# Performance work log

Measured on AMD Instinct MI355X. Metric: run time of the kernel, lower is better.

## Reference

```python
import jax, jax.numpy as jnp
import numpy as np

NUM_HEADS = 16

def setup_inputs() -> dict:
    key = jax.random.key(0)
    ks = jax.random.split(key, 5)
    N, T, D = 16, 4096, 1024
    # Linear weights stored as (in, out): y = x @ W + b (equivalent to torch x @ W.T + b)
    return {
        "x": jax.random.normal(ks[0], (N, T, D), jnp.float32),
        "w_qkv": jax.random.normal(ks[1], (D, 3 * D), jnp.float32) * (D ** -0.5),
        "b_qkv": jax.random.normal(ks[2], (3 * D,), jnp.float32) * 0.02,
        "w_proj": jax.random.normal(ks[3], (D, D), jnp.float32) * (D ** -0.5),
        "b_proj": jax.random.normal(ks[4], (D,), jnp.float32) * 0.02,
    }

def reference(x, w_qkv, b_qkv, w_proj, b_proj):
    N, T, D = x.shape
    H = NUM_HEADS
    hd = D // H
    scale = hd ** -0.5
    qkv = x @ w_qkv + b_qkv                      # (N,T,3D)
    qkv = qkv.reshape(N, T, 3, H, hd)
    q, k, v = qkv[:, :, 0], qkv[:, :, 1], qkv[:, :, 2]   # each (N,T,H,hd)
    # Faithful to source: matmul over last two dims -> scores across HEADS, (N,T,H,H)
    attn = jnp.einsum('nthd,ntgd->nthg', q * scale, k)
    attn = jax.nn.softmax(attn, axis=-1)
    out = jnp.einsum('nthg,ntgd->nthd', attn, v)         # (N,T,H,hd)
    # Faithful: transpose(2,1) then flatten -> (N,H,T,hd).reshape(N,T,D)
    out = out.transpose(0, 2, 1, 3).reshape(N, T, D)
    return out @ w_proj + b_proj
```

## Files before the change

### kernel.cpp

```cpp
#include <hip/hip_runtime.h>
#include <hip/hip_bf16.h>
#include <stdint.h>

typedef __bf16 bf16x8 __attribute__((ext_vector_type(8)));
typedef float f32x4 __attribute__((ext_vector_type(4)));
typedef unsigned short us8 __attribute__((ext_vector_type(8)));

__device__ __forceinline__ float bf2f(unsigned short u) {
    return __uint_as_float(((unsigned)u) << 16);
}
__device__ __forceinline__ unsigned short f2bf(float f) {
    __bf16 b = (__bf16)f;
    return __builtin_bit_cast(unsigned short, b);
}

__device__ __forceinline__ void gload16(const char* g, char* l) {
    __builtin_amdgcn_global_load_lds(
        (const __attribute__((address_space(1))) void*)g,
        (__attribute__((address_space(3))) void*)l, 16, 0, 0);
}

__global__ __launch_bounds__(256) void transpose_cast(
    const float* __restrict__ in, unsigned short* __restrict__ out,
    int K, int N)
{
    __shared__ float tile[32][33];
    const int tx = threadIdx.x, ty = threadIdx.y;
    const int n0 = blockIdx.x * 32, k0 = blockIdx.y * 32;
    #pragma unroll
    for (int i = 0; i < 32; i += 8)
        tile[ty + i][tx] = in[(long)(k0 + ty + i) * N + n0 + tx];
    __syncthreads();
    #pragma unroll
    for (int i = 0; i < 32; i += 8)
        out[(long)(n0 + ty + i) * K + k0 + tx] = f2bf(tile[tx][ty + i]);
}

__global__ __launch_bounds__(256) void cast_f32_bf16(
    const float* __restrict__ in, unsigned short* __restrict__ out, long n)
{
    const long stride = (long)gridDim.x * 256 * 8;
    for (long i = ((long)blockIdx.x * 256 + threadIdx.x) * 8; i < n; i += stride) {
        const f32x4 u0 = *(const f32x4*)&in[i];
        const f32x4 u1 = *(const f32x4*)&in[i + 4];
        us8 w;
        #pragma unroll
        for (int e = 0; e < 4; ++e) { w[e] = f2bf(u0[e]); w[e + 4] = f2bf(u1[e]); }
        *(us8*)&out[i] = w;
    }
}

#define MFMA16x16(a, b, c) __builtin_amdgcn_mfma_f32_16x16x32_bf16(a, b, c, 0, 0, 0)

#define PHASE_SYNC_PRE()                          \
    __builtin_amdgcn_sched_barrier(0);            \
    __builtin_amdgcn_s_barrier();                 \
    asm volatile("s_waitcnt lgkmcnt(0)");         \
    __builtin_amdgcn_sched_barrier(0);            \
    __builtin_amdgcn_s_setprio(1);

#define PHASE_SYNC_POST()                         \
    __builtin_amdgcn_s_setprio(0);                \
    __builtin_amdgcn_sched_barrier(0);            \
    __builtin_amdgcn_s_barrier();

#define TILE_BODY(T, BUFOFF)                                                     \
  do {                                                                           \
    const bool doStage = ((T) + 2 < KT);                                         \
    const long gk = (long)((T) + 2) * 128;                                       \
    bf16x8 alo[4][2], ahi[4][2], blo[2][2], bhi[2][2];                           \
                             \
    _Pragma("unroll")                                                            \
    for (int mi = 0; mi < 4; ++mi) {                                             \
        alo[mi][0] = *(const bf16x8*)(smem + (BUFOFF) + aBase + mi*2048 + k0);   \
        alo[mi][1] = *(const bf16x8*)(smem + (BUFOFF) + aBase + mi*2048 + k1);   \
    }                                                                            \
    _Pragma("unroll")                                                            \
    for (int ni = 0; ni < 2; ++ni) {                                             \
        blo[ni][0] = *(const bf16x8*)(smem + (BUFOFF) + bBase + ni*2048 + k0);   \
        blo[ni][1] = *(const bf16x8*)(smem + (BUFOFF) + bBase + ni*2048 + k1);   \
    }                                                                            \
    PHASE_SYNC_PRE()                                                             \
    _Pragma("unroll")                                                            \
    for (int mi = 0; mi < 4; ++mi)                                               \
        _Pragma("unroll")                                                        \
        for (int ni = 0; ni < 2; ++ni) {                                         \
            acc[mi][ni] = MFMA16x16(alo[mi][0], blo[ni][0], acc[mi][ni]);        \
            acc[mi][ni] = MFMA16x16(alo[mi][1], blo[ni][1], acc[mi][ni]);        \
        }                                                                        \
    PHASE_SYNC_POST()                                                            \
                     \
    _Pragma("unroll")                                                            \
    for (int mi = 0; mi < 4; ++mi) {                                             \
        ahi[mi][0] = *(const bf16x8*)(smem + (BUFOFF) + aBase + 8192 + mi*2048 + k0); \
        ahi[mi][1] = *(const bf16x8*)(smem + (BUFOFF) + aBase + 8192 + mi*2048 + k1); \
    }                                                                            \
    if (doStage) {                                                               \
        gload16(aStage + (long)(0*64)*Kb + gk, smem + (BUFOFF) + 0*8192 + ldsW); \
        gload16(aStage + (long)(2*64)*Kb + gk, smem + (BUFOFF) + 2*8192 + ldsW); \
    }                                                                            \
    PHASE_SYNC_PRE()                                                             \
    _Pragma("unroll")                                                            \
    for (int mi = 0; mi < 4; ++mi)                                               \
        _Pragma("unroll")                                                        \
        for (int ni = 0; ni < 2; ++ni) {                                         \
            acc[4+mi][ni] = MFMA16x16(ahi[mi][0], blo[ni][0], acc[4+mi][ni]);    \
            acc[4+mi][ni] = MFMA16x16(ahi[mi][1], blo[ni][1], acc[4+mi][ni]);    \
        }                                                                        \
    PHASE_SYNC_POST()                                                            \
                     \
    _Pragma("unroll")                                                            \
    for (int nj = 0; nj < 2; ++nj) {                                             \
        bhi[nj][0] = *(const bf16x8*)(smem + (BUFOFF) + bBase + (2+nj)*2048 + k0); \
        bhi[nj][1] = *(const bf16x8*)(smem + (BUFOFF) + bBase + (2+nj)*2048 + k1); \
    }                                                                            \
    if (doStage) {                                                               \
        gload16(aStage + (long)(1*64)*Kb + gk, smem + (BUFOFF) + 1*8192 + ldsW); \
        gload16(aStage + (long)(3*64)*Kb + gk, smem + (BUFOFF) + 3*8192 + ldsW); \
    }                                                                            \
    PHASE_SYNC_PRE()                                                             \
    _Pragma("unroll")                                                            \
    for (int mi = 0; mi < 4; ++mi)                                               \
        _Pragma("unroll")                                                        \
        for (int nj = 0; nj < 2; ++nj) {                                         \
            acc[mi][2+nj] = MFMA16x16(alo[mi][0], bhi[nj][0], acc[mi][2+nj]);    \
            acc[mi][2+nj] = MFMA16x16(alo[mi][1], bhi[nj][1], acc[mi][2+nj]);    \
        }                                                                        \
    PHASE_SYNC_POST()                                                            \
                \
    if (doStage) {                                                               \
        _Pragma("unroll")                                                        \
        for (int j = 0; j < 4; ++j)                                              \
            gload16(bStage + (long)(j*64)*Kb + gk,                               \
                    smem + (BUFOFF) + 32768 + j*8192 + ldsW);                    \
    }                                                                            \
    __builtin_amdgcn_sched_barrier(0);                                           \
    if (doStage) asm volatile("s_waitcnt vmcnt(8)");                             \
    else         asm volatile("s_waitcnt vmcnt(0)");                             \
    __builtin_amdgcn_sched_barrier(0);                                           \
    __builtin_amdgcn_s_barrier();                                                \
    __builtin_amdgcn_s_setprio(1);                                               \
    _Pragma("unroll")                                                            \
    for (int mi = 0; mi < 4; ++mi)                                               \
        _Pragma("unroll")                                                        \
        for (int nj = 0; nj < 2; ++nj) {                                         \
            acc[4+mi][2+nj] = MFMA16x16(ahi[mi][0], bhi[nj][0], acc[4+mi][2+nj]); \
            acc[4+mi][2+nj] = MFMA16x16(ahi[mi][1], bhi[nj][1], acc[4+mi][2+nj]); \
        }                                                                        \
    PHASE_SYNC_POST()                                                            \
  } while (0)

template<bool OUT_BF16>
__global__ __launch_bounds__(512, 2)
void gemm256(const unsigned short* __restrict__ A,
             const unsigned short* __restrict__ BT,
             const float* __restrict__ bias,
             void* __restrict__ Cp,
             int M, int N, int K)
{
    extern __shared__ char smem[];
    const int tid  = threadIdx.x;
    const int lane = tid & 63;
    const int w    = tid >> 6;
    const int wm   = w >> 2;
    const int wn   = w & 3;

    const int nwg  = gridDim.x;
    const int bid0 = blockIdx.x;
    const int bid  = (bid0 & 7) * (nwg >> 3) + (bid0 >> 3);
    const int nbx  = N >> 8;
    const int bx   = bid % nbx, by = bid / nbx;
    const long rowStart = (long)by * 256;
    const int  colStart = bx * 256;

    const int  KT = K >> 6;
    const long Kb = (long)K * 2;

    const int srow = w * 8 + (lane >> 3);
    const int scol = ((lane & 7) ^ (lane >> 3)) << 4;
    const char* aStage = (const char*)A  + (rowStart + srow) * Kb + scol;
    const char* bStage = (const char*)BT + ((long)colStart + srow) * Kb + scol;
    const int ldsW = w * 1024;

    const int fr = lane & 15;
    const int kq = lane >> 4;
    const int sw = (fr & 7) << 4;
    const int k0 = (kq * 16) ^ sw;
    const int k1 = (64 + kq * 16) ^ sw;
    const int aBase = (wm * 128 + fr) * 128;
    const int bBase = 32768 + (wn * 64 + fr) * 128;

    f32x4 acc[8][4] = {};

    #pragma unroll
    for (int tt = 0; tt < 2; ++tt) {
        #pragma unroll
        for (int j = 0; j < 4; ++j)
            gload16(aStage + (long)(j * 64) * Kb + (long)tt * 128,
                    smem + tt * 65536 + j * 8192 + ldsW);
        #pragma unroll
        for (int j = 0; j < 4; ++j)
            gload16(bStage + (long)(j * 64) * Kb + (long)tt * 128,
                    smem + tt * 65536 + 32768 + j * 8192 + ldsW);
    }
    asm volatile("s_waitcnt vmcnt(8)");
    __builtin_amdgcn_s_barrier();

    #pragma unroll 1
    for (int tp = 0; tp < KT / 2; ++tp) {
        TILE_BODY(2 * tp,     0);
        TILE_BODY(2 * tp + 1, 65536);
    }

    float bv[4];
    #pragma unroll
    for (int ni = 0; ni < 4; ++ni)
        bv[ni] = bias[colStart + wn * 64 + ni * 16 + fr];
    #pragma unroll
    for (int mi = 0; mi < 8; ++mi) {
        #pragma unroll
        for (int ni = 0; ni < 4; ++ni) {
            const int col = colStart + wn * 64 + ni * 16 + fr;
            #pragma unroll
            for (int e = 0; e < 4; ++e) {
                const long row = rowStart + wm * 128 + mi * 16 + kq * 4 + e;
                const float val = acc[mi][ni][e] + bv[ni];
                if constexpr (OUT_BF16)
                    ((unsigned short*)Cp)[row * N + col] = f2bf(val);
                else
                    ((float*)Cp)[row * N + col] = val;
            }
        }
    }
}

__global__ __launch_bounds__(256) void attn_kernel(
    const unsigned short* __restrict__ qkv, unsigned short* __restrict__ out)
{
    __shared__ unsigned short qkvs[4][3072];
    __shared__ float ps[4][256];
    __shared__ unsigned short os[4][1024];
    const int tid = threadIdx.x, lane = tid & 63, wave = tid >> 6;
    const long blockTok = (long)blockIdx.x * 4;

    const unsigned short* src = qkv + blockTok * 3072;
    unsigned short* dstBase = &qkvs[0][0];
    #pragma unroll
    for (int i = 0; i < 6; ++i) {
        const int o = (i * 256 + tid) * 8;
        *(us8*)&dstBase[o] = *(const us8*)&src[o];
    }
    __syncthreads();

    const unsigned short* q = &qkvs[wave][0];
    const unsigned short* kk = &qkvs[wave][1024];
    const unsigned short* vv = &qkvs[wave][2048];
    const int h = lane >> 2, g4 = lane & 3;

    float s[4] = {0.f, 0.f, 0.f, 0.f};
    #pragma unroll
    for (int d0 = 0; d0 < 64; d0 += 8) {
        const us8 q8 = *(const us8*)&q[h * 64 + d0];
        float qf[8];
        #pragma unroll
        for (int e = 0; e < 8; ++e) qf[e] = bf2f(q8[e]);
        #pragma unroll
        for (int j = 0; j < 4; ++j) {
            const us8 k8 = *(const us8*)&kk[(g4 * 4 + j) * 64 + d0];
            #pragma unroll
            for (int e = 0; e < 8; ++e) s[j] += qf[e] * bf2f(k8[e]);
        }
    }
    #pragma unroll
    for (int j = 0; j < 4; ++j) s[j] *= 0.125f;

    float mx = fmaxf(fmaxf(s[0], s[1]), fmaxf(s[2], s[3]));
    mx = fmaxf(mx, __shfl_xor(mx, 1, 64));
    mx = fmaxf(mx, __shfl_xor(mx, 2, 64));
    float p[4], sum = 0.f;
    #pragma unroll
    for (int j = 0; j < 4; ++j) { p[j] = expf(s[j] - mx); sum += p[j]; }
    sum += __shfl_xor(sum, 1, 64);
    sum += __shfl_xor(sum, 2, 64);
    const float inv = 1.f / sum;
    #pragma unroll
    for (int j = 0; j < 4; ++j) ps[wave][h * 16 + g4 * 4 + j] = p[j] * inv;
    __syncthreads();

    const int db = lane & 3;
    float o16[16] = {};
    #pragma unroll
    for (int gq = 0; gq < 4; ++gq) {
        const f32x4 pv = *(const f32x4*)&ps[wave][h * 16 + gq * 4];
        #pragma unroll
        for (int j = 0; j < 4; ++j) {
            const float pg = pv[j];
            const int g = gq * 4 + j;
            const us8 v8a = *(const us8*)&vv[g * 64 + db * 16];
            const us8 v8b = *(const us8*)&vv[g * 64 + db * 16 + 8];
            #pragma unroll
            for (int e = 0; e < 8; ++e) {
                o16[e]     += pg * bf2f(v8a[e]);
                o16[8 + e] += pg * bf2f(v8b[e]);
            }
        }
    }
    us8 w0, w1;
    #pragma unroll
    for (int e = 0; e < 8; ++e) { w0[e] = f2bf(o16[e]); w1[e] = f2bf(o16[8 + e]); }
    *(us8*)&os[wave][h * 64 + db * 16] = w0;
    *(us8*)&os[wave][h * 64 + db * 16 + 8] = w1;
    __syncthreads();

    #pragma unroll
    for (int i = 0; i < 2; ++i) {
        const int c = i * 256 + tid;
        const int w2 = c >> 7;
        const int cc = c & 127;
        const long m = blockTok + w2;
        const long n_ = m >> 12;
        const int t = (int)(m & 4095);
        const int hh = cc >> 3, slot = cc & 7;
        const long row = n_ * 4096 + hh * 256 + (t >> 4);
        const long colb = (long)(t & 15) * 128 + slot * 16;
        *(us8*)((char*)out + row * 2048 + colb) = *(const us8*)&os[w2][cc * 8];
    }
}

extern "C" void kernel_launch(void* const* d_in, const int* in_sizes, int n_in,
                              void* d_out, int out_size, void* d_ws, size_t ws_size,
                              hipStream_t stream) {
    const float* x      = (const float*)d_in[0];
    const float* w_qkv  = (const float*)d_in[1];
    const float* b_qkv  = (const float*)d_in[2];
    const float* w_proj = (const float*)d_in[3];
    const float* b_proj = (const float*)d_in[4];

    const long M = 65536;
    const size_t QKV_B = (size_t)M * 3072 * 2;
    const size_t XB_B  = (size_t)M * 1024 * 2;
    const size_t WQ_B  = 3072 * 1024 * 2;
    const size_t WP_B  = 1024 * 1024 * 2;
    if (ws_size < QKV_B + XB_B + WQ_B + WP_B) return;

    char* ws = (char*)d_ws;
    unsigned short* qkv    = (unsigned short*)ws;
    unsigned short* xb     = (unsigned short*)(ws + QKV_B);
    unsigned short* wqkvT  = (unsigned short*)(ws + QKV_B + XB_B);
    unsigned short* wprojT = (unsigned short*)(ws + QKV_B + XB_B + WQ_B);

    hipFuncSetAttribute((const void*)gemm256<true>,
                        hipFuncAttributeMaxDynamicSharedMemorySize, 131072);
    hipFuncSetAttribute((const void*)gemm256<false>,
                        hipFuncAttributeMaxDynamicSharedMemorySize, 131072);

    dim3 tb(32, 8);
    transpose_cast<<<dim3(3072 / 32, 1024 / 32), tb, 0, stream>>>(w_qkv, wqkvT, 1024, 3072);
    transpose_cast<<<dim3(1024 / 32, 1024 / 32), tb, 0, stream>>>(w_proj, wprojT, 1024, 1024);
    cast_f32_bf16<<<2048, 256, 0, stream>>>(x, xb, M * 1024);

    gemm256<true><<<dim3((3072 / 256) * (M / 256)), 512, 131072, stream>>>(
        xb, wqkvT, b_qkv, qkv, (int)M, 3072, 1024);

    attn_kernel<<<dim3(M / 4), 256, 0, stream>>>(qkv, xb);

    gemm256<false><<<dim3((1024 / 256) * (M / 256)), 512, 131072, stream>>>(
        xb, wprojT, b_proj, d_out, (int)M, 1024, 1024);
}
```

Before: 794.9 us.

## Prefetch next tile's LDS fragments across K-iterations with inline-asm ds_reads

Restructures the GEMM main loop so the A-lo and B-lo register fragments for the next K tile are read from the other LDS buffer during the current tile, instead of at its start. LDS reads become inline-asm ds_read_b128 with partial lgkmcnt waits, so MFMAs can begin before every fragment has arrived. Global-to-LDS staging waits are also moved earlier. This is meant to hide LDS read latency behind MFMA work. In exchange it keeps more fragment registers live across iterations and depends on hand-counted waitcnt values being exactly right.

```diff
diff --git a/kernel.cpp b/kernel.cpp
--- a/kernel.cpp
+++ b/kernel.cpp
@@ -18,6 +18,14 @@
     __builtin_amdgcn_global_load_lds(
         (const __attribute__((address_space(1))) void*)g,
         (__attribute__((address_space(3))) void*)l, 16, 0, 0);
+}
+
+__device__ __forceinline__ bf16x8 dsr128(const char* p) {
+    bf16x8 r;
+    asm volatile("ds_read_b128 %0, %1"
+                 : "=v"(r)
+                 : "v"((const __attribute__((address_space(3))) char*)p));
+    return r;
 }
 
 __global__ __launch_bounds__(256) void transpose_cast(
@@ -51,103 +59,90 @@
 }
 
 #define MFMA16x16(a, b, c) __builtin_amdgcn_mfma_f32_16x16x32_bf16(a, b, c, 0, 0, 0)
-
-#define PHASE_SYNC_PRE()                          \
-    __builtin_amdgcn_sched_barrier(0);            \
-    __builtin_amdgcn_s_barrier();                 \
-    asm volatile("s_waitcnt lgkmcnt(0)");         \
-    __builtin_amdgcn_sched_barrier(0);            \
-    __builtin_amdgcn_s_setprio(1);
-
-#define PHASE_SYNC_POST()                         \
-    __builtin_amdgcn_s_setprio(0);                \
-    __builtin_amdgcn_sched_barrier(0);            \
-    __builtin_amdgcn_s_barrier();
-
-#define TILE_BODY(T, BUFOFF)                                                     \
-  do {                                                                           \
-    const bool doStage = ((T) + 2 < KT);                                         \
-    const long gk = (long)((T) + 2) * 128;                                       \
-    bf16x8 alo[4][2], ahi[4][2], blo[2][2], bhi[2][2];                           \
-                             \
-    _Pragma("unroll")                                                            \
-    for (int mi = 0; mi < 4; ++mi) {                                             \
-        alo[mi][0] = *(const bf16x8*)(smem + (BUFOFF) + aBase + mi*2048 + k0);   \
-        alo[mi][1] = *(const bf16x8*)(smem + (BUFOFF) + aBase + mi*2048 + k1);   \
-    }                                                                            \
-    _Pragma("unroll")                                                            \
-    for (int ni = 0; ni < 2; ++ni) {                                             \
-        blo[ni][0] = *(const bf16x8*)(smem + (BUFOFF) + bBase + ni*2048 + k0);   \
-        blo[ni][1] = *(const bf16x8*)(smem + (BUFOFF) + bBase + ni*2048 + k1);   \
-    }                                                                            \
-    PHASE_SYNC_PRE()                                                             \
-    _Pragma("unroll")                                                            \
-    for (int mi = 0; mi < 4; ++mi)                                               \
-        _Pragma("unroll")                                                        \
-        for (int ni = 0; ni < 2; ++ni) {                                         \
-            acc[mi][ni] = MFMA16x16(alo[mi][0], blo[ni][0], acc[mi][ni]);        \
-            acc[mi][ni] = MFMA16x16(alo[mi][1], blo[ni][1], acc[mi][ni]);        \
-        }                                                                        \
-    PHASE_SYNC_POST()                                                            \
-                     \
-    _Pragma("unroll")                                                            \
-    for (int mi = 0; mi < 4; ++mi) {                                             \
-        ahi[mi][0] = *(const bf16x8*)(smem + (BUFOFF) + aBase + 8192 + mi*2048 + k0); \
-        ahi[mi][1] = *(const bf16x8*)(smem + (BUFOFF) + aBase + 8192 + mi*2048 + k1); \
-    }                                                                            \
-    if (doStage) {                                                               \
-        gload16(aStage + (long)(0*64)*Kb + gk, smem + (BUFOFF) + 0*8192 + ldsW); \
-        gload16(aStage + (long)(2*64)*Kb + gk, smem + (BUFOFF) + 2*8192 + ldsW); \
-    }                                                                            \
-    PHASE_SYNC_PRE()                                                             \
-    _Pragma("unroll")                                                            \
-    for (int mi = 0; mi < 4; ++mi)                                               \
-        _Pragma("unroll")                                                        \
-        for (int ni = 0; ni < 2; ++ni) {                                         \
-            acc[4+mi][ni] = MFMA16x16(ahi[mi][0], blo[ni][0], acc[4+mi][ni]);    \
-            acc[4+mi][ni] = MFMA16x16(ahi[mi][1], blo[ni][1], acc[4+mi][ni]);    \
-        }                                                                        \
-    PHASE_SYNC_POST()                                                            \
-                     \
-    _Pragma("unroll")                                                            \
-    for (int nj = 0; nj < 2; ++nj) {                                             \
-        bhi[nj][0] = *(const bf16x8*)(smem + (BUFOFF) + bBase + (2+nj)*2048 + k0); \
-        bhi[nj][1] = *(const bf16x8*)(smem + (BUFOFF) + bBase + (2+nj)*2048 + k1); \
-    }                                                                            \
-    if (doStage) {                                                               \
-        gload16(aStage + (long)(1*64)*Kb + gk, smem + (BUFOFF) + 1*8192 + ldsW); \
-        gload16(aStage + (long)(3*64)*Kb + gk, smem + (BUFOFF) + 3*8192 + ldsW); \
-    }                                                                            \
-    PHASE_SYNC_PRE()                                                             \
-    _Pragma("unroll")                                                            \
-    for (int mi = 0; mi < 4; ++mi)                                               \
-        _Pragma("unroll")                                                        \
-        for (int nj = 0; nj < 2; ++nj) {                                         \
-            acc[mi][2+nj] = MFMA16x16(alo[mi][0], bhi[nj][0], acc[mi][2+nj]);    \
-            acc[mi][2+nj] = MFMA16x16(alo[mi][1], bhi[nj][1], acc[mi][2+nj]);    \
-        }                                                                        \
-    PHASE_SYNC_POST()                                                            \
-                \
-    if (doStage) {                                                               \
-        _Pragma("unroll")                                                        \
-        for (int j = 0; j < 4; ++j)                                              \
-            gload16(bStage + (long)(j*64)*Kb + gk,                               \
-                    smem + (BUFOFF) + 32768 + j*8192 + ldsW);                    \
-    }                                                                            \
-    __builtin_amdgcn_sched_barrier(0);                                           \
-    if (doStage) asm volatile("s_waitcnt vmcnt(8)");                             \
-    else         asm volatile("s_waitcnt vmcnt(0)");                             \
-    __builtin_amdgcn_sched_barrier(0);                                           \
-    __builtin_amdgcn_s_barrier();                                                \
-    __builtin_amdgcn_s_setprio(1);                                               \
-    _Pragma("unroll")                                                            \
-    for (int mi = 0; mi < 4; ++mi)                                               \
-        _Pragma("unroll")                                                        \
-        for (int nj = 0; nj < 2; ++nj) {                                         \
-            acc[4+mi][2+nj] = MFMA16x16(ahi[mi][0], bhi[nj][0], acc[4+mi][2+nj]); \
-            acc[4+mi][2+nj] = MFMA16x16(ahi[mi][1], bhi[nj][1], acc[4+mi][2+nj]); \
-        }                                                                        \
-    PHASE_SYNC_POST()                                                            \
+#define SB __builtin_amdgcn_sched_barrier(0)
+#define BAR __builtin_amdgcn_s_barrier()
+
+#define MFMA_Q(AA, BB, RO, CO)                                                 \
+    _Pragma("unroll") for (int mi_ = 0; mi_ < 4; ++mi_)                        \
+        _Pragma("unroll") for (int ni_ = 0; ni_ < 2; ++ni_) {                  \
+            acc[(RO)+mi_][(CO)+ni_] =                                          \
+                MFMA16x16(AA[mi_][0], BB[ni_][0], acc[(RO)+mi_][(CO)+ni_]);    \
+            acc[(RO)+mi_][(CO)+ni_] =                                          \
+                MFMA16x16(AA[mi_][1], BB[ni_][1], acc[(RO)+mi_][(CO)+ni_]);    \
+        }
+
+#define TILE_BODY(T, BUF, OBUF)                                                \
+  do {                                                                         \
+    const bool sG = ((T) + 2 < KT);                                            \
+    const bool sR = ((T) + 1 < KT);                                            \
+    const long gk = (long)((T) + 2) * 128;                                     \
+                        \
+    _Pragma("unroll") for (int mi = 0; mi < 4; ++mi) {                         \
+        AHI[mi][0] = dsr128(smem + (BUF) + aBase + 8192 + mi*2048 + k0);       \
+        AHI[mi][1] = dsr128(smem + (BUF) + aBase + 8192 + mi*2048 + k1);       \
+    }                                                                          \
+    SB; BAR;                                                                   \
+    asm volatile("s_waitcnt lgkmcnt(8)");                                      \
+    SB;                                                                        \
+    __builtin_amdgcn_s_setprio(1);                                             \
+    MFMA_Q(ALO, BLO, 0, 0)                                                     \
+    __builtin_amdgcn_s_setprio(0);                                             \
+    SB; BAR;                                                                   \
+       \
+    _Pragma("unroll") for (int nj = 0; nj < 2; ++nj) {                         \
+        BHI[nj][0] = dsr128(smem + (BUF) + bBase + (2+nj)*2048 + k0);          \
+        BHI[nj][1] = dsr128(smem + (BUF) + bBase + (2+nj)*2048 + k1);          \
+    }                                                                          \
+    if (sG) {                                                                  \
+        gload16(aStage + (long)(0*64)*Kb + gk, smem + (BUF) + 0*8192 + ldsW);  \
+        gload16(aStage + (long)(2*64)*Kb + gk, smem + (BUF) + 2*8192 + ldsW);  \
+    }                                                                          \
+    SB;                                                                        \
+    if (sG) asm volatile("s_waitcnt vmcnt(2)");                                \
+    else    asm volatile("s_waitcnt vmcnt(0)");                                \
+    SB; BAR;                                                                   \
+    asm volatile("s_waitcnt lgkmcnt(4)");                                      \
+    SB;                                                                        \
+    __builtin_amdgcn_s_setprio(1);                                             \
+    MFMA_Q(AHI, BLO, 4, 0)                                                     \
+    __builtin_amdgcn_s_setprio(0);                                             \
+    SB; BAR;                                                                   \
+       \
+    if (sR) {                                                                  \
+        _Pragma("unroll") for (int ni = 0; ni < 2; ++ni) {                     \
+            BLO[ni][0] = dsr128(smem + (OBUF) + bBase + ni*2048 + k0);         \
+            BLO[ni][1] = dsr128(smem + (OBUF) + bBase + ni*2048 + k1);         \
+        }                                                                      \
+    }                                                                          \
+    if (sG) {                                                                  \
+        gload16(aStage + (long)(1*64)*Kb + gk, smem + (BUF) + 1*8192 + ldsW);  \
+        gload16(aStage + (long)(3*64)*Kb + gk, smem + (BUF) + 3*8192 + ldsW);  \
+    }                                                                          \
+    SB; BAR;                                                                   \
+    if (sR) asm volatile("s_waitcnt lgkmcnt(4)");                              \
+    else    asm volatile("s_waitcnt lgkmcnt(0)");                              \
+    SB;                                                                        \
+    __builtin_amdgcn_s_setprio(1);                                             \
+    MFMA_Q(ALO, BHI, 0, 2)                                                     \
+    __builtin_amdgcn_s_setprio(0);                                             \
+    SB; BAR;                                                                   \
+      \
+    if (sR) {                                                                  \
+        _Pragma("unroll") for (int mi = 0; mi < 4; ++mi) {                     \
+            ALO[mi][0] = dsr128(smem + (OBUF) + aBase + mi*2048 + k0);         \
+            ALO[mi][1] = dsr128(smem + (OBUF) + aBase + mi*2048 + k1);         \
+        }                                                                      \
+    }                                                                          \
+    if (sG) {                                                                  \
+        _Pragma("unroll") for (int j = 0; j < 4; ++j)                          \
+            gload16(bStage + (long)(j*64)*Kb + gk,                             \
+                    smem + (BUF) + 32768 + j*8192 + ldsW);                     \
+    }                                                                          \
+    SB; BAR; SB;                                                               \
+    __builtin_amdgcn_s_setprio(1);                                             \
+    MFMA_Q(AHI, BHI, 4, 2)                                                     \
+    __builtin_amdgcn_s_setprio(0);                                             \
+    SB; BAR;                                                                   \
   } while (0)
 
 template<bool OUT_BF16>
@@ -191,6 +186,7 @@
     const int bBase = 32768 + (wn * 64 + fr) * 128;
 
     f32x4 acc[8][4] = {};
+    bf16x8 ALO[4][2], AHI[4][2], BLO[2][2], BHI[2][2];
 
     #pragma unroll
     for (int tt = 0; tt < 2; ++tt) {
@@ -203,13 +199,28 @@
             gload16(bStage + (long)(j * 64) * Kb + (long)tt * 128,
                     smem + tt * 65536 + 32768 + j * 8192 + ldsW);
     }
+    SB;
     asm volatile("s_waitcnt vmcnt(8)");
-    __builtin_amdgcn_s_barrier();
+    SB; BAR;
+    #pragma unroll
+    for (int ni = 0; ni < 2; ++ni) {
+        BLO[ni][0] = dsr128(smem + bBase + ni*2048 + k0);
+        BLO[ni][1] = dsr128(smem + bBase + ni*2048 + k1);
+    }
+    #pragma unroll
+    for (int mi = 0; mi < 4; ++mi) {
+        ALO[mi][0] = dsr128(smem + aBase + mi*2048 + k0);
+        ALO[mi][1] = dsr128(smem + aBase + mi*2048 + k1);
+    }
+    asm volatile("s_waitcnt lgkmcnt(0)");
+    SB;
 
     #pragma unroll 1
     for (int tp = 0; tp < KT / 2; ++tp) {
-        TILE_BODY(2 * tp,     0);
-        TILE_BODY(2 * tp + 1, 65536);
+        TILE_BODY(2 * tp,     0,     65536);
+        TILE_BODY(2 * tp + 1, 65536, 0);
+        asm volatile("s_waitcnt lgkmcnt(0)");
+        SB;
     }
 
     float bv[4];
```

After: 1.093 ms. +37.5%, slower.
